# Kernel optimization log

Hardware: AMD Instinct MI355X
Metric: run time of the kernel (lower is better)

Reference implementation:

```python
import jax, jax.numpy as jnp
import numpy as np

C, H, W = 64, 32, 32
N = 32
HW = H * W
EPS = 1e-5


def setup_inputs() -> dict:
    kk = jax.random.key(0)
    ks = jax.random.split(kk, 6)
    shp = (N, C, H, W)
    return {
        "query": jax.random.normal(ks[0], shp, jnp.float32),
        "key": jax.random.normal(ks[1], shp, jnp.float32),
        "value": jax.random.normal(ks[2], shp, jnp.float32),
        "ln1_w": jnp.ones((C, H, W), jnp.float32),
        "ln1_b": jnp.zeros((C, H, W), jnp.float32),
        "ln2_w": jnp.ones((C, H, W), jnp.float32),
        "ln2_b": jnp.zeros((C, H, W), jnp.float32),
        "ln3_w": jnp.ones((C, H, W), jnp.float32),
        "ln3_b": jnp.zeros((C, H, W), jnp.float32),
        "wq": jax.random.normal(ks[3], (C, C), jnp.float32) / np.sqrt(C).astype(np.float32),
        "bq": jnp.zeros((C,), jnp.float32),
        "wk": jax.random.normal(ks[4], (C, C), jnp.float32) / np.sqrt(C).astype(np.float32),
        "bk": jnp.zeros((C,), jnp.float32),
        "wv": jax.random.normal(ks[5], (C, C), jnp.float32) / np.sqrt(C).astype(np.float32),
        "bv": jnp.zeros((C,), jnp.float32),
    }


def _ln(x, w, b):
    # LayerNorm over the full (C,H,W) normalized_shape, as nn.LayerNorm(dim)
    mu = jnp.mean(x, axis=(1, 2, 3), keepdims=True)
    var = jnp.var(x, axis=(1, 2, 3), keepdims=True)
    return (x - mu) * jax.lax.rsqrt(var + EPS) * w + b


def _proj(x, w, b):
    # 1x1 conv == per-pixel channel mixing; output reshaped to (N, C, H*W)
    y = jnp.einsum('oc,nchw->nohw', w, x) + b[None, :, None, None]
    return y.reshape(x.shape[0], C, HW)


def reference(query, key, value, ln1_w, ln1_b, ln2_w, ln2_b, ln3_w, ln3_b,
              wq, bq, wk, bk, wv, bv):
    qn = _ln(query, ln1_w, ln1_b)
    kn = _ln(key, ln2_w, ln2_b)
    vn = _ln(value, ln3_w, ln3_b)
    q = _proj(qn, wq, bq)   # (N, C, HW)
    k = _proj(kn, wk, bk)
    v = _proj(vn, wv, bv)
    # attention[n,i,j] = sum_c k[n,c,i] * q[n,c,j] / sqrt(C); softmax over dim=1 (i)
    attn = jnp.einsum('nci,ncj->nij', k, q) / jnp.sqrt(jnp.float32(C))
    attn = jax.nn.softmax(attn, axis=1)
    # output = v @ attn : (N, C, HW)
    out = jnp.einsum('nci,nij->ncj', v, attn).reshape(qn.shape)
    # residual adds the NORMALIZED query (that's what SelfAttention receives)
    x = (qn + out).reshape(qn.shape[0], -1)  # (N, C*H*W)
    return x, attn
```

## Files before the change

### kernel.cpp

```cpp
#include <hip/hip_runtime.h>
#include <math.h>

#define NB   32
#define CCH  64
#define HWD  1024
#define CHW  65536
#define EPSV 1e-5f

typedef __attribute__((ext_vector_type(8))) short bf16x8;
typedef __attribute__((ext_vector_type(4))) float f32x4;

__device__ __forceinline__ unsigned f2b(float x) {
    union { float f; unsigned u; } v; v.f = x;
    return (v.u + 0x7fffu + ((v.u >> 16) & 1u)) >> 16;
}
__device__ __forceinline__ float b2f(unsigned short u) {
    union { unsigned u; float f; } v; v.u = ((unsigned)u) << 16;
    return v.f;
}

__global__ __launch_bounds__(256)
void k_stats(const float* __restrict__ q, const float* __restrict__ k,
             const float* __restrict__ v, float* __restrict__ part)
{
    const int chunk = blockIdx.x, which = blockIdx.y, n = blockIdx.z;
    const float* x = (which == 0) ? q : (which == 1 ? k : v);
    const float4* x4 = (const float4*)(x + (size_t)n * CHW) + chunk * 2048;
    float s = 0.f, ss = 0.f;
#pragma unroll
    for (int i = 0; i < 8; ++i) {
        float4 t = x4[threadIdx.x + i * 256];
        s  += t.x + t.y + t.z + t.w;
        ss += t.x * t.x + t.y * t.y + t.z * t.z + t.w * t.w;
    }
    __shared__ float rs[256], rss[256];
    rs[threadIdx.x] = s; rss[threadIdx.x] = ss;
    __syncthreads();
    for (int off = 128; off > 0; off >>= 1) {
        if (threadIdx.x < off) {
            rs[threadIdx.x]  += rs[threadIdx.x + off];
            rss[threadIdx.x] += rss[threadIdx.x + off];
        }
        __syncthreads();
    }
    if (threadIdx.x == 0) {
        const int b = (n * 3 + which) * 8 + chunk;
        part[b * 2 + 0] = rs[0];
        part[b * 2 + 1] = rss[0];
    }
}

__global__ __launch_bounds__(256, 4)
void k_proj(const float* __restrict__ q,  const float* __restrict__ k,  const float* __restrict__ v,
            const float* __restrict__ w1, const float* __restrict__ b1,
            const float* __restrict__ w2, const float* __restrict__ b2,
            const float* __restrict__ w3, const float* __restrict__ b3,
            const float* __restrict__ wq, const float* __restrict__ bq,
            const float* __restrict__ wk, const float* __restrict__ bk,
            const float* __restrict__ wv, const float* __restrict__ bv,
            const float* __restrict__ part,
            float* __restrict__ qn, short* __restrict__ pqt,
            short* __restrict__ pkt, short* __restrict__ pvb)
{
    __shared__ short xnb[64][72];
    __shared__ float musd[6];
    const int pt = blockIdx.x, n = blockIdx.y;
    const int t = threadIdx.x;
    const int w = t >> 6, l = t & 63;
    const int l15 = l & 15, lg = l >> 4;

    if (t < 3) {
        float s = 0.f, ss = 0.f;
#pragma unroll
        for (int cidx = 0; cidx < 8; ++cidx) {
            const int b = (n * 3 + t) * 8 + cidx;
            s  += part[b * 2 + 0];
            ss += part[b * 2 + 1];
        }
        const float mu = s * (1.0f / CHW);
        musd[t * 2 + 0] = mu;
        musd[t * 2 + 1] = rsqrtf(ss * (1.0f / CHW) - mu * mu + EPSV);
    }
    __syncthreads();

    const float* src[3]   = {q, k, v};
    const float* lw[3]    = {w1, w2, w3};
    const float* lb[3]    = {b1, b2, b3};
    const float* pw[3]    = {wq, wk, wv};
    const float* pbias[3] = {bq, bk, bv};

    for (int tt = 0; tt < 3; ++tt) {
        const float sc = (tt == 0) ? 0.125f : 1.0f;

        bf16x8 whi[2], wlo[2];
#pragma unroll
        for (int ks = 0; ks < 2; ++ks) {
            float wf[8];
            *(float4*)&wf[0] = *(const float4*)&pw[tt][(w * 16 + l15) * 64 + ks * 32 + lg * 8];
            *(float4*)&wf[4] = *(const float4*)&pw[tt][(w * 16 + l15) * 64 + ks * 32 + lg * 8 + 4];
#pragma unroll
            for (int e = 0; e < 8; ++e) {
                const float ws = wf[e] * sc;
                const unsigned hi = f2b(ws);
                whi[ks][e] = (short)hi;
                wlo[ks][e] = (short)f2b(ws - b2f((unsigned short)hi));
            }
        }

        const float mu = musd[tt * 2], is = musd[tt * 2 + 1];
        for (int idx = t; idx < 1024; idx += 256) {
            const int c = idx >> 4, p4 = idx & 15;
            const int gi = c * HWD + pt * 64 + p4 * 4;
            float4 xv = *(const float4*)&src[tt][(size_t)n * CHW + gi];
            float4 w4 = *(const float4*)&lw[tt][gi];
            float4 b4 = *(const float4*)&lb[tt][gi];
            float4 r;
            r.x = (xv.x - mu) * is * w4.x + b4.x;
            r.y = (xv.y - mu) * is * w4.y + b4.y;
            r.z = (xv.z - mu) * is * w4.z + b4.z;
            r.w = (xv.w - mu) * is * w4.w + b4.w;
            if (tt == 0) *(float4*)&qn[(size_t)n * CHW + gi] = r;
            xnb[p4 * 4 + 0][c] = (short)f2b(r.x);
            xnb[p4 * 4 + 1][c] = (short)f2b(r.y);
            xnb[p4 * 4 + 2][c] = (short)f2b(r.z);
            xnb[p4 * 4 + 3][c] = (short)f2b(r.w);
        }
        __syncthreads();

        if (tt < 2) {
            const float4 bb = *(const float4*)&pbias[tt][w * 16 + lg * 4];
            short* dst = (tt == 0) ? pqt : pkt;
#pragma unroll
            for (int pt4 = 0; pt4 < 4; ++pt4) {
                f32x4 acc = {};
#pragma unroll
                for (int ks = 0; ks < 2; ++ks) {
                    bf16x8 xb = *(const bf16x8*)&xnb[pt4 * 16 + l15][ks * 32 + lg * 8];
                    acc = __builtin_amdgcn_mfma_f32_16x16x32_bf16(whi[ks], xb, acc, 0, 0, 0);
                    acc = __builtin_amdgcn_mfma_f32_16x16x32_bf16(wlo[ks], xb, acc, 0, 0, 0);
                }
                const int pix = pt * 64 + pt4 * 16 + l15;
                uint2 u;
                u.x = (f2b(acc[1] + bb.y * sc) << 16) | f2b(acc[0] + bb.x * sc);
                u.y = (f2b(acc[3] + bb.w * sc) << 16) | f2b(acc[2] + bb.z * sc);
                *(uint2*)&dst[(size_t)n * CHW + pix * 64 + w * 16 + lg * 4] = u;
            }
        } else {
            const float bo = pbias[2][w * 16 + l15];
#pragma unroll
            for (int pt4 = 0; pt4 < 4; ++pt4) {
                f32x4 acc = {};
#pragma unroll
                for (int ks = 0; ks < 2; ++ks) {
                    bf16x8 xb = *(const bf16x8*)&xnb[pt4 * 16 + l15][ks * 32 + lg * 8];
                    acc = __builtin_amdgcn_mfma_f32_16x16x32_bf16(xb, whi[ks], acc, 0, 0, 0);
                    acc = __builtin_amdgcn_mfma_f32_16x16x32_bf16(xb, wlo[ks], acc, 0, 0, 0);
                }
                const int o   = w * 16 + l15;
                const int px4 = pt * 64 + pt4 * 16 + lg * 4;
                uint2 u;
                u.x = (f2b(acc[1] + bo) << 16) | f2b(acc[0] + bo);
                u.y = (f2b(acc[3] + bo) << 16) | f2b(acc[2] + bo);
                *(uint2*)&pvb[(size_t)n * CHW + o * HWD + px4] = u;
            }
        }
        __syncthreads();
    }
}

__global__ __launch_bounds__(512, 4)
void k_attn3(const short* __restrict__ pqt, const short* __restrict__ pkt,
             const short* __restrict__ pvb, const float* __restrict__ qn,
             float* __restrict__ xout, float* __restrict__ attn)
{
    __shared__ __align__(16) char smem[65536 + 4608 + 2048];
    short* q_lds = (short*)(smem + 65536);
    float* wredM = (float*)(smem + 65536 + 4608);
    float* wredS = wredM + 256;

    const int wg  = blockIdx.x;
    const int xcd = wg & 7, lid = wg >> 3;
    const int n   = xcd * 4 + (lid >> 5);
    const int jb  = lid & 31;
    const size_t nb = (size_t)n * CHW;
    const int t = threadIdx.x;
    const int w = t >> 6;
    const int l = t & 63;
    const int l15 = l & 15, lg = l >> 4;
    const int ibase = w * 128;

    if (t < 256) {
        const int j = t >> 3, c8 = (t & 7) * 8;
        *(bf16x8*)&q_lds[j * 72 + c8] =
            *(const bf16x8*)&pqt[nb + (size_t)(jb * 32 + j) * 64 + c8];
    }
    __syncthreads();

    f32x4 acc[8][2] = {};
#pragma unroll
    for (int ks = 0; ks < 2; ++ks) {
        bf16x8 bqf[2];
#pragma unroll
        for (int jt = 0; jt < 2; ++jt)
            bqf[jt] = *(const bf16x8*)&q_lds[(jt * 16 + l15) * 72 + ks * 32 + lg * 8];
#pragma unroll
        for (int f = 0; f < 8; ++f) {
            const int i = ibase + f * 16 + l15;
            bf16x8 af = *(const bf16x8*)&pkt[nb + (size_t)i * 64 + ks * 32 + lg * 8];
#pragma unroll
            for (int jt = 0; jt < 2; ++jt)
                acc[f][jt] = __builtin_amdgcn_mfma_f32_16x16x32_bf16(
                    af, bqf[jt], acc[f][jt], 0, 0, 0);
        }
    }

    float mself[2];
#pragma unroll
    for (int jt = 0; jt < 2; ++jt) {
        float m = -1e30f;
#pragma unroll
        for (int f = 0; f < 8; ++f)
#pragma unroll
            for (int r = 0; r < 4; ++r) m = fmaxf(m, acc[f][jt][r]);
        m = fmaxf(m, __shfl_xor(m, 16));
        m = fmaxf(m, __shfl_xor(m, 32));
        mself[jt] = m;
        float s = 0.f;
#pragma unroll
        for (int f = 0; f < 8; ++f)
#pragma unroll
            for (int r = 0; r < 4; ++r) {
                float e = __expf(acc[f][jt][r] - m);
                acc[f][jt][r] = e;
                s += e;
            }
        s += __shfl_xor(s, 16);
        s += __shfl_xor(s, 32);
        if (l < 16) {
            wredM[w * 32 + jt * 16 + l] = m;
            wredS[w * 32 + jt * 16 + l] = s;
        }
    }
    __syncthreads();

#pragma unroll
    for (int jt = 0; jt < 2; ++jt) {
        const int j = jt * 16 + l15;
        float M = wredM[j];
#pragma unroll
        for (int ww = 1; ww < 8; ++ww) M = fmaxf(M, wredM[ww * 32 + j]);
        float S = 0.f;
#pragma unroll
        for (int ww = 0; ww < 8; ++ww)
            S += wredS[ww * 32 + j] * __expf(wredM[ww * 32 + j] - M);
        const float fac = __expf(mself[jt] - M) / S;
#pragma unroll
        for (int f = 0; f < 8; ++f) {
            const int i0 = ibase + f * 16 + lg * 4;
            uint2 pw;
            pw.x = (f2b(acc[f][jt][1] * fac) << 16) | f2b(acc[f][jt][0] * fac);
            pw.y = (f2b(acc[f][jt][3] * fac) << 16) | f2b(acc[f][jt][2] * fac);
            const unsigned byte = (unsigned)j * 2048u + (((unsigned)i0 * 2u) ^ (((unsigned)j & 7u) << 4));
            *(uint2*)(smem + byte) = pw;
        }
    }
    __syncthreads();

    if (w < 4) {
        f32x4 oacc[2] = {};
        __builtin_amdgcn_s_setprio(1);
#pragma unroll 4
        for (int ks = 0; ks < 32; ++ks) {
            bf16x8 av = *(const bf16x8*)&pvb[nb + (size_t)(w * 16 + l15) * HWD + ks * 32 + lg * 8];
            const unsigned ib = (unsigned)(ks * 32 + lg * 8) * 2u;
#pragma unroll
            for (int u = 0; u < 2; ++u) {
                const int j = u * 16 + l15;
                bf16x8 bp = *(const bf16x8*)(smem + (unsigned)j * 2048u + (ib ^ (((unsigned)j & 7u) << 4)));
                oacc[u] = __builtin_amdgcn_mfma_f32_16x16x32_bf16(av, bp, oacc[u], 0, 0, 0);
            }
        }
        __builtin_amdgcn_s_setprio(0);
#pragma unroll
        for (int u = 0; u < 2; ++u) {
            const int j = u * 16 + l15;
#pragma unroll
            for (int r = 0; r < 4; ++r) {
                const int c = w * 16 + lg * 4 + r;
                const size_t o = nb + (size_t)c * HWD + jb * 32 + j;
                xout[o] = oacc[u][r] + qn[o];
            }
        }
    } else {
        float* aout = attn + (size_t)n * HWD * HWD + jb * 32;
        const int jq   = (l & 7) * 4;
        const int isub = l >> 3;
        const int i00  = (w - 4) * 256;
#pragma unroll 4
        for (int g = 0; g < 32; ++g) {
            const int i = i00 + g * 8 + isub;
            f32x4 o4;
#pragma unroll
            for (int r = 0; r < 4; ++r) {
                const unsigned j = (unsigned)(jq + r);
                const unsigned byte = j * 2048u + (((unsigned)i * 2u) ^ ((j & 7u) << 4));
                o4[r] = b2f(*(const unsigned short*)(smem + byte));
            }
            *(f32x4*)&aout[(size_t)i * HWD + jq] = o4;
        }
    }
}

extern "C" void kernel_launch(void* const* d_in, const int* in_sizes, int n_in,
                              void* d_out, int out_size, void* d_ws, size_t ws_size,
                              hipStream_t stream)
{
    const float* q  = (const float*)d_in[0];
    const float* k  = (const float*)d_in[1];
    const float* v  = (const float*)d_in[2];
    const float* w1 = (const float*)d_in[3];
    const float* b1 = (const float*)d_in[4];
    const float* w2 = (const float*)d_in[5];
    const float* b2 = (const float*)d_in[6];
    const float* w3 = (const float*)d_in[7];
    const float* b3 = (const float*)d_in[8];
    const float* wq = (const float*)d_in[9];
    const float* bq = (const float*)d_in[10];
    const float* wk = (const float*)d_in[11];
    const float* bk = (const float*)d_in[12];
    const float* wv = (const float*)d_in[13];
    const float* bv = (const float*)d_in[14];

    float* ws   = (float*)d_ws;
    float* part = ws;
    float* qn   = ws + 4096;
    short* pqt  = (short*)(qn + 2097152);
    short* pkt  = pqt + 2097152;
    short* pvb  = pkt + 2097152;

    float* xout = (float*)d_out;
    float* attn = xout + 2097152;

    k_stats<<<dim3(8, 3, 32), 256, 0, stream>>>(q, k, v, part);
    k_proj<<<dim3(16, 32), 256, 0, stream>>>(q, k, v, w1, b1, w2, b2, w3, b3,
                                             wq, bq, wk, bk, wv, bv,
                                             part, qn, pqt, pkt, pvb);
    k_attn3<<<dim3(1024), dim3(512), 0, stream>>>(pqt, pkt, pvb, qn, xout, attn);
}
```

Before: 73.24 us.

## Widen attention tile to 64 query columns per 1024-thread block

The attention kernel now gives each block 64 query columns instead of 32, using 1024 threads and about 148KB of LDS. Each K slab read from global memory now serves twice as many columns, and the attention-matrix output rows become 256-byte contiguous float stores instead of 128-byte ones. The LDS read order in the writeback loop is rotated per lane group to reduce bank conflicts. In exchange, only one block fits per CU and the grid is halved to 512 blocks, which may hurt latency hiding and load balance.

```diff
diff --git a/kernel.cpp b/kernel.cpp
--- a/kernel.cpp
+++ b/kernel.cpp
@@ -168,31 +168,33 @@
     }
 }
 
-__global__ __launch_bounds__(512, 4)
-void k_attn3(const short* __restrict__ pqt, const short* __restrict__ pkt,
+__global__ __launch_bounds__(1024, 1)
+void k_attn4(const short* __restrict__ pqt, const short* __restrict__ pkt,
              const short* __restrict__ pvb, const float* __restrict__ qn,
              float* __restrict__ xout, float* __restrict__ attn)
 {
-    __shared__ __align__(16) char smem[65536 + 4608 + 2048];
-    short* q_lds = (short*)(smem + 65536);
-    float* wredM = (float*)(smem + 65536 + 4608);
-    float* wredS = wredM + 256;
+    __shared__ __align__(16) char smem[131072 + 9216 + 8192];
+    short* q_lds = (short*)(smem + 131072);
+    float* wredM = (float*)(smem + 131072 + 9216);
+    float* wredS = wredM + 1024;
 
     const int wg  = blockIdx.x;
     const int xcd = wg & 7, lid = wg >> 3;
-    const int n   = xcd * 4 + (lid >> 5);
-    const int jb  = lid & 31;
+    const int n   = xcd * 4 + (lid >> 4);
+    const int jb  = lid & 15;
     const size_t nb = (size_t)n * CHW;
     const int t = threadIdx.x;
     const int w = t >> 6;
     const int l = t & 63;
     const int l15 = l & 15, lg = l >> 4;
-    const int ibase = w * 128;
-
-    if (t < 256) {
+    const int jh    = w & 1;
+    const int islab = w >> 1;
+    const int ibase = islab * 128;
+
+    if (t < 512) {
         const int j = t >> 3, c8 = (t & 7) * 8;
         *(bf16x8*)&q_lds[j * 72 + c8] =
-            *(const bf16x8*)&pqt[nb + (size_t)(jb * 32 + j) * 64 + c8];
+            *(const bf16x8*)&pqt[nb + (size_t)(jb * 64 + j) * 64 + c8];
     }
     __syncthreads();
 
@@ -202,7 +204,7 @@
         bf16x8 bqf[2];
 #pragma unroll
         for (int jt = 0; jt < 2; ++jt)
-            bqf[jt] = *(const bf16x8*)&q_lds[(jt * 16 + l15) * 72 + ks * 32 + lg * 8];
+            bqf[jt] = *(const bf16x8*)&q_lds[(jh * 32 + jt * 16 + l15) * 72 + ks * 32 + lg * 8];
 #pragma unroll
         for (int f = 0; f < 8; ++f) {
             const int i = ibase + f * 16 + l15;
@@ -237,22 +239,23 @@
         s += __shfl_xor(s, 16);
         s += __shfl_xor(s, 32);
         if (l < 16) {
-            wredM[w * 32 + jt * 16 + l] = m;
-            wredS[w * 32 + jt * 16 + l] = s;
+            wredM[w * 64 + jh * 32 + jt * 16 + l] = m;
+            wredS[w * 64 + jh * 32 + jt * 16 + l] = s;
         }
     }
     __syncthreads();
 
 #pragma unroll
     for (int jt = 0; jt < 2; ++jt) {
-        const int j = jt * 16 + l15;
-        float M = wredM[j];
-#pragma unroll
-        for (int ww = 1; ww < 8; ++ww) M = fmaxf(M, wredM[ww * 32 + j]);
+        const int jgl = jh * 32 + jt * 16 + l15;
+        float M = wredM[jh * 64 + jgl];
+#pragma unroll
+        for (int s8 = 1; s8 < 8; ++s8)
+            M = fmaxf(M, wredM[(2 * s8 + jh) * 64 + jgl]);
         float S = 0.f;
 #pragma unroll
-        for (int ww = 0; ww < 8; ++ww)
-            S += wredS[ww * 32 + j] * __expf(wredM[ww * 32 + j] - M);
+        for (int s8 = 0; s8 < 8; ++s8)
+            S += wredS[(2 * s8 + jh) * 64 + jgl] * __expf(wredM[(2 * s8 + jh) * 64 + jgl] - M);
         const float fac = __expf(mself[jt] - M) / S;
 #pragma unroll
         for (int f = 0; f < 8; ++f) {
@@ -260,22 +263,23 @@
             uint2 pw;
             pw.x = (f2b(acc[f][jt][1] * fac) << 16) | f2b(acc[f][jt][0] * fac);
             pw.y = (f2b(acc[f][jt][3] * fac) << 16) | f2b(acc[f][jt][2] * fac);
-            const unsigned byte = (unsigned)j * 2048u + (((unsigned)i0 * 2u) ^ (((unsigned)j & 7u) << 4));
+            const unsigned byte = (unsigned)jgl * 2048u + (((unsigned)i0 * 2u) ^ (((unsigned)jgl & 7u) << 4));
             *(uint2*)(smem + byte) = pw;
         }
     }
     __syncthreads();
 
-    if (w < 4) {
+    if (w < 8) {
+        const int cm = w & 3, jh2 = w >> 2;
         f32x4 oacc[2] = {};
         __builtin_amdgcn_s_setprio(1);
 #pragma unroll 4
         for (int ks = 0; ks < 32; ++ks) {
-            bf16x8 av = *(const bf16x8*)&pvb[nb + (size_t)(w * 16 + l15) * HWD + ks * 32 + lg * 8];
+            bf16x8 av = *(const bf16x8*)&pvb[nb + (size_t)(cm * 16 + l15) * HWD + ks * 32 + lg * 8];
             const unsigned ib = (unsigned)(ks * 32 + lg * 8) * 2u;
 #pragma unroll
             for (int u = 0; u < 2; ++u) {
-                const int j = u * 16 + l15;
+                const int j = jh2 * 32 + u * 16 + l15;
                 bf16x8 bp = *(const bf16x8*)(smem + (unsigned)j * 2048u + (ib ^ (((unsigned)j & 7u) << 4)));
                 oacc[u] = __builtin_amdgcn_mfma_f32_16x16x32_bf16(av, bp, oacc[u], 0, 0, 0);
             }
@@ -283,28 +287,30 @@
         __builtin_amdgcn_s_setprio(0);
 #pragma unroll
         for (int u = 0; u < 2; ++u) {
-            const int j = u * 16 + l15;
+            const int j = jh2 * 32 + u * 16 + l15;
 #pragma unroll
             for (int r = 0; r < 4; ++r) {
-                const int c = w * 16 + lg * 4 + r;
-                const size_t o = nb + (size_t)c * HWD + jb * 32 + j;
+                const int c = cm * 16 + lg * 4 + r;
+                const size_t o = nb + (size_t)c * HWD + jb * 64 + j;
                 xout[o] = oacc[u][r] + qn[o];
             }
         }
     } else {
-        float* aout = attn + (size_t)n * HWD * HWD + jb * 32;
-        const int jq   = (l & 7) * 4;
-        const int isub = l >> 3;
-        const int i00  = (w - 4) * 256;
+        float* aout = attn + (size_t)n * HWD * HWD + jb * 64;
+        const int ww   = w - 8;
+        const int jq   = (l & 15) * 4;
+        const int isub = l >> 4;
+        const int i00  = ww * 128;
 #pragma unroll 4
         for (int g = 0; g < 32; ++g) {
-            const int i = i00 + g * 8 + isub;
+            const int i = i00 + g * 4 + isub;
             f32x4 o4;
 #pragma unroll
-            for (int r = 0; r < 4; ++r) {
-                const unsigned j = (unsigned)(jq + r);
+            for (int rr = 0; rr < 4; ++rr) {
+                const int rro = (rr + isub) & 3;
+                const unsigned j = (unsigned)(jq + rro);
                 const unsigned byte = j * 2048u + (((unsigned)i * 2u) ^ ((j & 7u) << 4));
-                o4[r] = b2f(*(const unsigned short*)(smem + byte));
+                o4[rro] = b2f(*(const unsigned short*)(smem + byte));
             }
             *(f32x4*)&aout[(size_t)i * HWD + jq] = o4;
         }
@@ -345,5 +351,5 @@
     k_proj<<<dim3(16, 32), 256, 0, stream>>>(q, k, v, w1, b1, w2, b2, w3, b3,
                                              wq, bq, wk, bk, wv, bv,
                                              part, qn, pqt, pkt, pvb);
-    k_attn3<<<dim3(1024), dim3(512), 0, stream>>>(pqt, pkt, pvb, qn, xout, attn);
-}
+    k_attn4<<<dim3(512), dim3(1024), 0, stream>>>(pqt, pkt, pvb, qn, xout, attn);
+}
```

Result: slower. 78.32 us (+6.9%).
